# Kernel optimization log

Hardware: AMD Instinct MI355X
Metric: run time of the kernel (lower is better)

## Reference

```python
import jax, jax.numpy as jnp
import numpy as np

NUM_GRAPHS = 512
EPS = 1e-5

def squash(x):
    # capsule squash: (|x|^2 / (1 + |x|^2)) * x / |x|
    n2 = jnp.sum(x * x, axis=-1, keepdims=True)
    return (n2 / (1.0 + n2)) * x * jax.lax.rsqrt(n2 + 1e-12)

def setup_inputs():
    key = jax.random.key(0)
    ks = jax.random.split(key, 16)
    N, E, F, H, L, C = 100000, 600000, 128, 128, 3, 2
    x = jax.random.normal(ks[0], (N, F), jnp.float32)
    edge_index = jax.random.randint(ks[1], (2, E), 0, N)
    batch = jnp.sort(jax.random.randint(ks[2], (N,), 0, NUM_GRAPHS))
    def lin(k, i, o):
        return (jax.random.normal(k, (i, o), jnp.float32) / np.sqrt(i)).astype(jnp.float32)
    return {
        'x': x, 'edge_index': edge_index, 'batch': batch,
        'bn_gamma': jnp.ones((F,), jnp.float32), 'bn_beta': jnp.zeros((F,), jnp.float32),
        'W0': lin(ks[3], F, H), 'b0': jnp.zeros((H,), jnp.float32),
        'W1': lin(ks[4], H, H), 'b1': jnp.zeros((H,), jnp.float32),
        'W2': lin(ks[5], H, H), 'b2': jnp.zeros((H,), jnp.float32),
        'tar_w': (jax.random.normal(ks[6], (L, H), jnp.float32) / np.sqrt(H)).astype(jnp.float32),
        'lin1_w': lin(ks[7], 3 * H, H), 'lin1_b': jnp.zeros((H,), jnp.float32),
        'lin2_w': lin(ks[8], H, C), 'lin2_b': jnp.zeros((C,), jnp.float32),
    }

def reference(x, edge_index, batch, bn_gamma, bn_beta, W0, b0, W1, b1, W2, b2,
              tar_w, lin1_w, lin1_b, lin2_w, lin2_b):
    N, G = x.shape[0], NUM_GRAPHS
    # input BatchNorm1d (training-mode batch statistics)
    mu = jnp.mean(x, 0)
    var = jnp.var(x, 0)
    h = (x - mu) * jax.lax.rsqrt(var + EPS) * bn_gamma + bn_beta
    # remove_self_loops + add_remaining_self_loops ~= append diagonal with weight 1
    loops = jnp.arange(N)
    src = jnp.concatenate([edge_index[0], loops])
    dst = jnp.concatenate([edge_index[1], loops])
    w = jnp.ones((src.shape[0],), h.dtype)
    # GCN symmetric normalization D^-1/2 A D^-1/2
    deg = jax.ops.segment_sum(w, dst, num_segments=N)
    dinv = jax.lax.rsqrt(jnp.maximum(deg, 1e-12))
    norm = dinv[src] * w * dinv[dst]  # [E+N]
    ones_n = jnp.ones((N,), h.dtype)
    cnt = jax.ops.segment_sum(ones_n, batch, num_segments=G)  # nodes per graph
    cnt_safe = jnp.maximum(cnt, 1.0)[:, None]
    graph_rep = jnp.zeros((G, 3 * W0.shape[1]), h.dtype)
    loss_stability = jnp.zeros((), h.dtype)
    for i, (W, b) in enumerate([(W0, b0), (W1, b1), (W2, b2)]):
        m = h @ W  # [N, H]
        agg = jax.ops.segment_sum(norm[:, None] * m[src], dst, num_segments=N) + b
        h = squash(agg)
        loss_stability = loss_stability + jnp.mean((agg - h) ** 2)
        # Task-Aware Readout: node attention then fused sum / mean / max scatters
        attn = h @ tar_w[i]  # [N]
        x_wsum = jax.ops.segment_sum(attn[:, None] * h, batch, num_segments=G)
        x_mean = jax.ops.segment_sum(h, batch, num_segments=G) / cnt_safe
        x_max = jax.ops.segment_max(h, batch, num_segments=G)
        x_max = jnp.where(cnt[:, None] > 0, x_max, 0.0)
        graph_rep = graph_rep + jnp.concatenate([x_wsum, x_mean, x_max], axis=-1)
    z = jax.nn.relu(graph_rep @ lin1_w + lin1_b)
    z = z @ lin2_w + lin2_b
    return jax.nn.log_softmax(z, axis=-1)
```

## Files before the change

kernel.cpp:

```cpp
#include <hip/hip_runtime.h>
#include <hip/hip_bf16.h>
#include <math.h>

#define BN_EPS 1e-5f
#define NCHUNK 256

typedef __attribute__((ext_vector_type(8)))  short short8v;
typedef __attribute__((ext_vector_type(16))) float f32x16;

__device__ __forceinline__ unsigned short f2bf(float f){
  union { float f; unsigned u; } v; v.f = f;
  unsigned r = v.u + 0x7FFFu + ((v.u >> 16) & 1u);
  return (unsigned short)(r >> 16);
}
__device__ __forceinline__ float2 bfpair(unsigned u){
  union { unsigned u; float f; } lo, hi;
  lo.u = u << 16;
  hi.u = u & 0xFFFF0000u;
  return make_float2(lo.f, hi.f);
}
__device__ __forceinline__ unsigned packbf(float a, float b){
  return (unsigned)f2bf(a) | ((unsigned)f2bf(b) << 16);
}

__global__ __launch_bounds__(256) void k_hist_bn(const int* __restrict__ dst,
                                                 int* __restrict__ hist2, int E, int NB, int CH,
                                                 const float* __restrict__ x,
                                                 float* __restrict__ part, int total4){
  int tid = threadIdx.x;
  if (blockIdx.x < NCHUNK){
    __shared__ int lh[512];
    for (int i = tid; i < NB; i += 256) lh[i] = 0;
    __syncthreads();
    int c = blockIdx.x;
    int e0 = c*CH, e1 = min(e0 + CH, E);
    for (int e = e0 + tid; e < e1; e += 256)
      atomicAdd(&lh[dst[e] >> 8], 1);
    __syncthreads();
    for (int i = tid; i < NB; i += 256)
      hist2[c*NB + i] = lh[i];
  } else {
    const float4* x4 = (const float4*)x;
    int bb = blockIdx.x - NCHUNK;
    int stride = 512 * 256;
    float4 s = make_float4(0.f,0.f,0.f,0.f);
    float4 q = make_float4(0.f,0.f,0.f,0.f);
    for (int idx = bb*256 + tid; idx < total4; idx += stride){
      float4 v = x4[idx];
      s.x += v.x; s.y += v.y; s.z += v.z; s.w += v.w;
      q.x += v.x*v.x; q.y += v.y*v.y; q.z += v.z*v.z; q.w += v.w*v.w;
    }
    __shared__ float4 shs[256], shq[256];
    shs[tid] = s; shq[tid] = q;
    __syncthreads();
    if (tid < 32){
      int c4 = tid;
      float4 ts = shs[c4], tq = shq[c4];
      #pragma unroll
      for (int j = 1; j < 8; ++j){
        float4 os = shs[c4 + j*32], oq = shq[c4 + j*32];
        ts.x += os.x; ts.y += os.y; ts.z += os.z; ts.w += os.w;
        tq.x += oq.x; tq.y += oq.y; tq.z += oq.z; tq.w += oq.w;
      }
      float* pb = part + (size_t)bb * 256;
      *(float4*)(pb + c4*4)       = ts;
      *(float4*)(pb + 128 + c4*4) = tq;
    }
  }
}

__global__ __launch_bounds__(512) void k_scan_red_gb(const int* __restrict__ hist2,
                                                     int* __restrict__ offs2,
                                                     int* __restrict__ bbase, int NB, int E,
                                                     const float* __restrict__ part,
                                                     const float* __restrict__ gamma,
                                                     const float* __restrict__ beta,
                                                     float* __restrict__ scale,
                                                     float* __restrict__ shift, int N,
                                                     const int* __restrict__ batch,
                                                     int* __restrict__ gstart, int G){
  int t = threadIdx.x;
  if (blockIdx.x == 0){
    __shared__ int tot[512];
    int b = t;
    int total = 0;
    if (b < NB){
      for (int c = 0; c < NCHUNK; c += 8){
        int h0 = hist2[(c+0)*NB + b], h1 = hist2[(c+1)*NB + b];
        int h2 = hist2[(c+2)*NB + b], h3 = hist2[(c+3)*NB + b];
        int h4 = hist2[(c+4)*NB + b], h5 = hist2[(c+5)*NB + b];
        int h6 = hist2[(c+6)*NB + b], h7 = hist2[(c+7)*NB + b];
        total += ((h0+h1)+(h2+h3)) + ((h4+h5)+(h6+h7));
      }
    }
    tot[b] = (b < NB) ? total : 0;
    __syncthreads();
    int v = tot[b];
    for (int d = 1; d < 512; d <<= 1){
      int u = (b >= d) ? tot[b-d] : 0;
      __syncthreads();
      tot[b] += u;
      __syncthreads();
    }
    if (b < NB){
      int base = tot[b] - v;
      bbase[b] = base;
      int run = base;
      for (int c = 0; c < NCHUNK; ++c){
        offs2[c*NB + b] = run;
        run += hist2[c*NB + b];
      }
    }
    if (b == 0) bbase[NB] = E;
  } else if (blockIdx.x == 1){
    if (t < 256){
      float a0=0.f,a1=0.f,a2=0.f,a3=0.f,a4=0.f,a5=0.f,a6=0.f,a7=0.f;
      for (int b = 0; b < 512; b += 8){
        a0 += part[(size_t)(b+0)*256 + t];
        a1 += part[(size_t)(b+1)*256 + t];
        a2 += part[(size_t)(b+2)*256 + t];
        a3 += part[(size_t)(b+3)*256 + t];
        a4 += part[(size_t)(b+4)*256 + t];
        a5 += part[(size_t)(b+5)*256 + t];
        a6 += part[(size_t)(b+6)*256 + t];
        a7 += part[(size_t)(b+7)*256 + t];
      }
      float acc = ((a0+a1)+(a2+a3)) + ((a4+a5)+(a6+a7));
      __shared__ float sh[256];
      sh[t] = acc;
      __syncthreads();
      if (t < 128){
        float mu  = sh[t] / (float)N;
        float var = sh[t+128] / (float)N - mu*mu;
        float sc  = gamma[t] * rsqrtf(var + BN_EPS);
        scale[t] = sc;
        shift[t] = beta[t] - mu*sc;
      }
    }
  } else {
    int g = (blockIdx.x - 2)*512 + t;
    if (g <= G){
      int lo = 0, hi = N;
      while (lo < hi){ int mid = (lo+hi)>>1; if (batch[mid] < g) lo = mid+1; else hi = mid; }
      gstart[g] = lo;
    }
  }
}

__global__ __launch_bounds__(256) void chunk_scatter(const int* __restrict__ src,
                                                     const int* __restrict__ dst,
                                                     const int* __restrict__ offs2,
                                                     unsigned* __restrict__ ebuf,
                                                     int E, int NB, int CH){
  __shared__ int lcur[512];
  int c = blockIdx.x;
  for (int i = threadIdx.x; i < NB; i += 256) lcur[i] = offs2[c*NB + i];
  __syncthreads();
  int e0 = c*CH, e1 = min(e0 + CH, E);
  for (int e = e0 + threadIdx.x; e < e1; e += 256){
    int d = dst[e];
    int b = d >> 8;
    int pos = atomicAdd(&lcur[b], 1);
    ebuf[pos] = ((unsigned)(d & 255) << 24) | (unsigned)src[e];
  }
}

__global__ __launch_bounds__(256) void k_sort_prep(const unsigned* __restrict__ ebuf,
                                                   const int* __restrict__ bbase,
                                                   int* __restrict__ csrs,
                                                   int* __restrict__ rowstart,
                                                   float* __restrict__ dinv,
                                                   int N, int E, int NB,
                                                   const float* __restrict__ W0,
                                                   const float* __restrict__ W1,
                                                   const float* __restrict__ W2,
                                                   const float* __restrict__ scale,
                                                   unsigned short* __restrict__ Wh,
                                                   const float* __restrict__ b0,
                                                   const float* __restrict__ shift,
                                                   float* __restrict__ bias0p){
  int tid = threadIdx.x;
  if ((int)blockIdx.x < NB){
    int b = blockIdx.x;
    int base = bbase[b];
    int end  = bbase[b+1];
    int len  = end - base;
    __shared__ int cnt[256];
    __shared__ int pref[256];
    cnt[tid] = 0;
    __syncthreads();
    for (int i = tid; i < len; i += 256)
      atomicAdd(&cnt[ebuf[base + i] >> 24], 1);
    __syncthreads();
    int v = cnt[tid];
    pref[tid] = v;
    __syncthreads();
    for (int d = 1; d < 256; d <<= 1){
      int u = (tid >= d) ? pref[tid-d] : 0;
      __syncthreads();
      pref[tid] += u;
      __syncthreads();
    }
    int excl = pref[tid] - v;
    int node = b*256 + tid;
    if (node < N){
      rowstart[node] = base + excl;
      dinv[node] = rsqrtf((float)v + 1.0f);
    }
    cnt[tid] = excl;
    __syncthreads();
    for (int i = tid; i < len; i += 256){
      unsigned r = ebuf[base + i];
      int pos = atomicAdd(&cnt[r >> 24], 1);
      csrs[base + pos] = (int)(r & 0xFFFFFFu);
    }
    if (b == NB-1 && tid == 0) rowstart[N] = E;
  } else if ((int)blockIdx.x < NB + 192){
    int idx = (blockIdx.x - NB)*256 + tid;
    int l = idx >> 14, r = idx & 16383, c = r >> 7, k = r & 127;
    const float* W = (l==0) ? W0 : (l==1) ? W1 : W2;
    float v = W[k*128 + c];
    if (l == 0) v *= scale[k];
    Wh[idx] = f2bf(v);
  } else {
    __shared__ float sh[128];
    if (tid < 128) sh[tid] = shift[tid];
    __syncthreads();
    if (tid < 128){
      float s = b0[tid];
      for (int c = 0; c < 128; ++c) s += sh[c] * W0[c*128 + tid];
      bias0p[tid] = s;
    }
  }
}

template<int CVT>
__global__ __launch_bounds__(512) void gemm_mfma(
    const float* __restrict__ A32, const unsigned short* __restrict__ A16,
    const unsigned short* __restrict__ Bh, unsigned short* __restrict__ C, int N){
  __shared__ unsigned short Ah[64*128];
  int tid = threadIdx.x;
  int r0 = blockIdx.x * 64;
  int w = tid >> 6, lane = tid & 63;
  int rt = w & 1;
  int ct = (w >> 1) * 32;
  int lrow = 32*rt + (lane & 31);
  int khalf = lane >> 5;
  int c0 = ct + (lane & 31);
  const unsigned short* bh0 = Bh + (size_t)c0*128 + khalf*8;

  short8v bhf[8];
  #pragma unroll
  for (int s = 0; s < 8; ++s) bhf[s] = *(const short8v*)(bh0 + s*16);

  if (CVT){
    #pragma unroll
    for (int it = 0; it < 4; ++it){
      int idx = tid + it*512;
      int row = idx >> 5;
      int c4  = idx & 31;
      int r = r0 + row;
      float4 av = (r < N) ? *(const float4*)(A32 + (size_t)r*128 + c4*4)
                          : make_float4(0.f,0.f,0.f,0.f);
      int byte0 = (c4*8) ^ ((row & 15) << 4);
      uint2 p = make_uint2(packbf(av.x, av.y), packbf(av.z, av.w));
      *(uint2*)((char*)Ah + row*256 + byte0) = p;
    }
  } else {
    #pragma unroll
    for (int it = 0; it < 2; ++it){
      int idx = tid + it*512;
      int row = idx >> 4;
      int c8  = idx & 15;
      int r = r0 + row;
      uint4 v = (r < N) ? *(const uint4*)(A16 + (size_t)r*128 + c8*8)
                        : make_uint4(0,0,0,0);
      int byte0 = (c8*16) ^ ((row & 15) << 4);
      *(uint4*)((char*)Ah + row*256 + byte0) = v;
    }
  }
  __syncthreads();

  f32x16 acc = {};
  const char* AhB = (const char*)Ah + lrow*256;
  int sw = (lrow & 15) << 4;
  #pragma unroll
  for (int s = 0; s < 8; ++s){
    int abyte = (s*32 + khalf*16) ^ sw;
    short8v a = *(const short8v*)(AhB + abyte);
    acc = __builtin_amdgcn_mfma_f32_32x32x16_bf16(a, bhf[s], acc, 0, 0, 0);
  }

  #pragma unroll
  for (int r = 0; r < 16; ++r){
    int row = r0 + 32*rt + (r & 3) + 8*(r >> 2) + 4*khalf;
    if (row < N) C[(size_t)row*128 + c0] = f2bf(acc[r]);
  }
}

__global__ __launch_bounds__(256) void gather_squash(
    const unsigned short* __restrict__ m, const int* __restrict__ rowstart,
    const int* __restrict__ csrs, const float* __restrict__ dinv,
    const float* __restrict__ bias, const float* __restrict__ tar,
    unsigned short* __restrict__ h, float* __restrict__ attn, int N){
  int node = blockIdx.x*8 + (threadIdx.x >> 5);
  if (node >= N) return;
  int lane = threadIdx.x & 31;
  const uint2* m2 = (const uint2*)m;
  float dv = dinv[node];
  float sn = dv*dv;
  uint2 sv = m2[(size_t)node*32 + lane];
  float2 p0 = bfpair(sv.x), p1 = bfpair(sv.y);
  float a0 = p0.x*sn, a1 = p0.y*sn, a2 = p1.x*sn, a3 = p1.y*sn;
  int j0 = rowstart[node], j1 = rowstart[node+1];

  for (int base = j0; base < j1; base += 32){
    int cnt = j1 - base; if (cnt > 32) cnt = 32;
    int sidx = 0; float swt = 0.f;
    if (lane < cnt){
      sidx = csrs[base + lane];
      swt  = dinv[sidx] * dv;
    }
    int t = 0;
    for (; t + 4 <= cnt; t += 4){
      int s0 = __shfl(sidx, t, 32),   s1 = __shfl(sidx, t+1, 32);
      int s2 = __shfl(sidx, t+2, 32), s3 = __shfl(sidx, t+3, 32);
      float w0 = __shfl(swt, t, 32),   w1 = __shfl(swt, t+1, 32);
      float w2 = __shfl(swt, t+2, 32), w3 = __shfl(swt, t+3, 32);
      uint2 u0 = m2[(size_t)s0*32 + lane];
      uint2 u1 = m2[(size_t)s1*32 + lane];
      uint2 u2 = m2[(size_t)s2*32 + lane];
      uint2 u3 = m2[(size_t)s3*32 + lane];
      float2 q0, q1;
      q0 = bfpair(u0.x); q1 = bfpair(u0.y);
      a0 += w0*q0.x; a1 += w0*q0.y; a2 += w0*q1.x; a3 += w0*q1.y;
      q0 = bfpair(u1.x); q1 = bfpair(u1.y);
      a0 += w1*q0.x; a1 += w1*q0.y; a2 += w1*q1.x; a3 += w1*q1.y;
      q0 = bfpair(u2.x); q1 = bfpair(u2.y);
      a0 += w2*q0.x; a1 += w2*q0.y; a2 += w2*q1.x; a3 += w2*q1.y;
      q0 = bfpair(u3.x); q1 = bfpair(u3.y);
      a0 += w3*q0.x; a1 += w3*q0.y; a2 += w3*q1.x; a3 += w3*q1.y;
    }
    if (cnt - t >= 2){
      int s0 = __shfl(sidx, t, 32), s1 = __shfl(sidx, t+1, 32);
      float w0 = __shfl(swt, t, 32), w1 = __shfl(swt, t+1, 32);
      uint2 u0 = m2[(size_t)s0*32 + lane];
      uint2 u1 = m2[(size_t)s1*32 + lane];
      float2 q0 = bfpair(u0.x), q1 = bfpair(u0.y);
      a0 += w0*q0.x; a1 += w0*q0.y; a2 += w0*q1.x; a3 += w0*q1.y;
      q0 = bfpair(u1.x); q1 = bfpair(u1.y);
      a0 += w1*q0.x; a1 += w1*q0.y; a2 += w1*q1.x; a3 += w1*q1.y;
      t += 2;
    }
    if (t < cnt){
      int s0 = __shfl(sidx, t, 32);
      float w0 = __shfl(swt, t, 32);
      uint2 u0 = m2[(size_t)s0*32 + lane];
      float2 q0 = bfpair(u0.x), q1 = bfpair(u0.y);
      a0 += w0*q0.x; a1 += w0*q0.y; a2 += w0*q1.x; a3 += w0*q1.y;
    }
  }

  float4 bv = ((const float4*)bias)[lane];
  a0 += bv.x; a1 += bv.y; a2 += bv.z; a3 += bv.w;
  float n2 = a0*a0 + a1*a1 + a2*a2 + a3*a3;
  #pragma unroll
  for (int o = 16; o > 0; o >>= 1) n2 += __shfl_xor(n2, o);
  float sc = (n2/(1.f+n2)) * rsqrtf(n2 + 1e-12f);
  float h0 = a0*sc, h1 = a1*sc, h2 = a2*sc, h3 = a3*sc;
  ((uint2*)(h + (size_t)node*128))[lane] = make_uint2(packbf(h0,h1), packbf(h2,h3));
  float4 tv = ((const float4*)tar)[lane];
  float at = h0*tv.x + h1*tv.y + h2*tv.z + h3*tv.w;
  #pragma unroll
  for (int o = 16; o > 0; o >>= 1) at += __shfl_xor(at, o);
  if (lane == 0) attn[node] = at;
}

__global__ __launch_bounds__(1024) void readout(const unsigned short* __restrict__ h,
                                                const float* __restrict__ attn,
                                                const int* __restrict__ gstart,
                                                float* __restrict__ grep){
  int g = blockIdx.x;
  int t   = threadIdx.x & 63;
  int grp = threadIdx.x >> 6;
  int a = gstart[g], b = gstart[g+1];
  float wsx = 0.f, wsy = 0.f, smx_ = 0.f, smy_ = 0.f;
  float mxx = -INFINITY, mxy = -INFINITY;
  for (int n = a + grp; n < b; n += 16){
    unsigned u = ((const unsigned*)(h + (size_t)n*128))[t];
    float2 v = bfpair(u);
    float at = attn[n];
    wsx += at*v.x; wsy += at*v.y;
    smx_ += v.x;  smy_ += v.y;
    mxx = fmaxf(mxx, v.x); mxy = fmaxf(mxy, v.y);
  }
  __shared__ float2 sws[16][64], ssm[16][64], smx[16][64];
  sws[grp][t] = make_float2(wsx, wsy);
  ssm[grp][t] = make_float2(smx_, smy_);
  smx[grp][t] = make_float2(mxx, mxy);
  __syncthreads();
  if (grp == 0){
    #pragma unroll
    for (int j = 1; j < 16; ++j){
      float2 ow = sws[j][t], os = ssm[j][t], om = smx[j][t];
      wsx += ow.x; wsy += ow.y;
      smx_ += os.x; smy_ += os.y;
      mxx = fmaxf(mxx, om.x); mxy = fmaxf(mxy, om.y);
    }
    int cnt = b - a;
    float inv = 1.f / fmaxf((float)cnt, 1.f);
    if (cnt == 0){ mxx = 0.f; mxy = 0.f; }
    grep[(size_t)g*384 + t*2]           += wsx;
    grep[(size_t)g*384 + t*2 + 1]       += wsy;
    grep[(size_t)g*384 + 128 + t*2]     += smx_*inv;
    grep[(size_t)g*384 + 128 + t*2 + 1] += smy_*inv;
    grep[(size_t)g*384 + 256 + t*2]     += mxx;
    grep[(size_t)g*384 + 256 + t*2 + 1] += mxy;
  }
}

__global__ __launch_bounds__(128) void classify(const float* __restrict__ grep,
                                                const float* __restrict__ w1, const float* __restrict__ b1,
                                                const float* __restrict__ w2, const float* __restrict__ b2,
                                                float* __restrict__ out){
  int g = blockIdx.x, t = threadIdx.x;
  __shared__ float gr[384];
  for (int i = t; i < 384; i += 128) gr[i] = grep[(size_t)g*384 + i];
  __syncthreads();
  float z = b1[t];
  for (int k = 0; k < 384; ++k) z += gr[k]*w1[k*128 + t];
  z = fmaxf(z, 0.f);
  float c0 = z*w2[t*2 + 0], c1 = z*w2[t*2 + 1];
  #pragma unroll
  for (int o = 32; o > 0; o >>= 1){ c0 += __shfl_xor(c0, o); c1 += __shfl_xor(c1, o); }
  __shared__ float r0s[2], r1s[2];
  if ((t & 63) == 0){ r0s[t>>6] = c0; r1s[t>>6] = c1; }
  __syncthreads();
  if (t == 0){
    float z0 = r0s[0] + r0s[1] + b2[0];
    float z1 = r1s[0] + r1s[1] + b2[1];
    float mm = fmaxf(z0, z1);
    float lse = mm + logf(expf(z0-mm) + expf(z1-mm));
    out[g*2 + 0] = z0 - lse;
    out[g*2 + 1] = z1 - lse;
  }
}

extern "C" void kernel_launch(void* const* d_in, const int* in_sizes, int n_in,
                              void* d_out, int out_size, void* d_ws, size_t ws_size,
                              hipStream_t stream) {
  const float* x     = (const float*)d_in[0];
  const int*   ei    = (const int*)d_in[1];
  const int*   batch = (const int*)d_in[2];
  const float* gamma = (const float*)d_in[3];
  const float* beta  = (const float*)d_in[4];
  const float* W0    = (const float*)d_in[5];
  const float* b0    = (const float*)d_in[6];
  const float* W1    = (const float*)d_in[7];
  const float* b1    = (const float*)d_in[8];
  const float* W2    = (const float*)d_in[9];
  const float* b2    = (const float*)d_in[10];
  const float* tar   = (const float*)d_in[11];
  const float* l1w   = (const float*)d_in[12];
  const float* l1b   = (const float*)d_in[13];
  const float* l2w   = (const float*)d_in[14];
  const float* l2b   = (const float*)d_in[15];
  float* out = (float*)d_out;

  int N = in_sizes[0] / 128;
  int E = in_sizes[1] / 2;
  int G = out_size / 2;
  const int* srcp = ei;
  const int* dstp = ei + E;

  char* wsb = (char*)d_ws;
  size_t off = 0;
  auto alloc = [&](size_t bytes)->char*{
    char* p = wsb + off; off += (bytes + 255) & ~(size_t)255; return p;
  };
  unsigned short* h = (unsigned short*)alloc((size_t)N*128*2);
  unsigned short* m = (unsigned short*)alloc((size_t)N*128*2);
  float* attn    = (float*)alloc((size_t)N*4);
  float* dinv    = (float*)alloc((size_t)N*4);
  int*   rowst   = (int*)  alloc((size_t)(N+1)*4);
  int*   csrs    = (int*)  alloc((size_t)E*4);
  unsigned* ebuf = (unsigned*)alloc((size_t)E*4);
  int*   hist2   = (int*)  alloc((size_t)NCHUNK*512*4);
  int*   offs2   = (int*)  alloc((size_t)NCHUNK*512*4);
  int*   bbase   = (int*)  alloc(513*4);
  int*   gstart  = (int*)  alloc((size_t)(G+1)*4);
  float* grep    = (float*)alloc((size_t)G*384*4);
  float* stats   = (float*)alloc(2*128*4);
  float* bias0p  = (float*)alloc(128*4);
  float* part    = (float*)alloc((size_t)512*256*4);
  unsigned short* Wh = (unsigned short*)alloc(3*16384*2);
  (void)ws_size;

  float* scale  = stats;
  float* shift  = stats + 128;

  int NB = (N + 255) >> 8;
  int CH = (E + NCHUNK - 1) / NCHUNK;
  hipMemsetAsync(grep, 0, (size_t)G*384*4, stream);

  k_hist_bn<<<NCHUNK + 512, 256, 0, stream>>>(dstp, hist2, E, NB, CH, x, part, N*32);
  k_scan_red_gb<<<4, 512, 0, stream>>>(hist2, offs2, bbase, NB, E,
                                       part, gamma, beta, scale, shift, N,
                                       batch, gstart, G);
  chunk_scatter<<<NCHUNK, 256, 0, stream>>>(srcp, dstp, offs2, ebuf, E, NB, CH);
  k_sort_prep<<<NB + 193, 256, 0, stream>>>(ebuf, bbase, csrs, rowst, dinv, N, E, NB,
                                            W0, W1, W2, scale, Wh, b0, shift, bias0p);

  const float* bs[3] = {bias0p, b1, b2};
  int nb64 = (N + 63) / 64;
  for (int l = 0; l < 3; ++l){
    if (l == 0)
      gemm_mfma<1><<<nb64, 512, 0, stream>>>(x, nullptr, Wh, m, N);
    else
      gemm_mfma<0><<<nb64, 512, 0, stream>>>(nullptr, h, Wh + l*16384, m, N);
    gather_squash<<<(N+7)/8, 256, 0, stream>>>(m, rowst, csrs, dinv, bs[l], tar + l*128, h, attn, N);
    readout<<<G, 1024, 0, stream>>>(h, attn, gstart, grep);
  }
  classify<<<G, 128, 0, stream>>>(grep, l1w, l1b, l2w, l2b, out);
}
```

Baseline: 252.4 us.

## Merge independent kernels into shared launches to cut launch count

Launches that do not depend on each other now share one kernel and branch on block index. The grep memset moves into the histogram/BN kernel, and the weight conversion joins chunk_scatter. The CSR sort runs in the same launch as the layer-0 GEMM, and each readout is fused with the next layer's GEMM. This removes several launches and lets independent work overlap, at the cost of mixed block types, larger shared memory per block, and an 8-group readout instead of 16.

```diff
diff --git a/kernel.cpp b/kernel.cpp
--- a/kernel.cpp
+++ b/kernel.cpp
@@ -23,10 +23,157 @@
   return (unsigned)f2bf(a) | ((unsigned)f2bf(b) << 16);
 }
 
-__global__ __launch_bounds__(256) void k_hist_bn(const int* __restrict__ dst,
-                                                 int* __restrict__ hist2, int E, int NB, int CH,
-                                                 const float* __restrict__ x,
-                                                 float* __restrict__ part, int total4){
+
+template<int CVT>
+__device__ __forceinline__ void gemm_body(int bid, int tid,
+    const float* __restrict__ A32, const unsigned short* __restrict__ A16,
+    const unsigned short* __restrict__ Bh, unsigned short* __restrict__ C, int N,
+    unsigned short* Ah){
+  int r0 = bid * 64;
+  int w = tid >> 6, lane = tid & 63;
+  int rt = w & 1;
+  int ct = (w >> 1) * 32;
+  int lrow = 32*rt + (lane & 31);
+  int khalf = lane >> 5;
+  int c0 = ct + (lane & 31);
+  const unsigned short* bh0 = Bh + (size_t)c0*128 + khalf*8;
+
+  short8v bhf[8];
+  #pragma unroll
+  for (int s = 0; s < 8; ++s) bhf[s] = *(const short8v*)(bh0 + s*16);
+
+  if (CVT){
+    #pragma unroll
+    for (int it = 0; it < 4; ++it){
+      int idx = tid + it*512;
+      int row = idx >> 5;
+      int c4  = idx & 31;
+      int r = r0 + row;
+      float4 av = (r < N) ? *(const float4*)(A32 + (size_t)r*128 + c4*4)
+                          : make_float4(0.f,0.f,0.f,0.f);
+      int byte0 = (c4*8) ^ ((row & 15) << 4);
+      uint2 p = make_uint2(packbf(av.x, av.y), packbf(av.z, av.w));
+      *(uint2*)((char*)Ah + row*256 + byte0) = p;
+    }
+  } else {
+    #pragma unroll
+    for (int it = 0; it < 2; ++it){
+      int idx = tid + it*512;
+      int row = idx >> 4;
+      int c8  = idx & 15;
+      int r = r0 + row;
+      uint4 v = (r < N) ? *(const uint4*)(A16 + (size_t)r*128 + c8*8)
+                        : make_uint4(0,0,0,0);
+      int byte0 = (c8*16) ^ ((row & 15) << 4);
+      *(uint4*)((char*)Ah + row*256 + byte0) = v;
+    }
+  }
+  __syncthreads();
+
+  f32x16 acc = {};
+  const char* AhB = (const char*)Ah + lrow*256;
+  int sw = (lrow & 15) << 4;
+  #pragma unroll
+  for (int s = 0; s < 8; ++s){
+    int abyte = (s*32 + khalf*16) ^ sw;
+    short8v a = *(const short8v*)(AhB + abyte);
+    acc = __builtin_amdgcn_mfma_f32_32x32x16_bf16(a, bhf[s], acc, 0, 0, 0);
+  }
+
+  #pragma unroll
+  for (int r = 0; r < 16; ++r){
+    int row = r0 + 32*rt + (r & 3) + 8*(r >> 2) + 4*khalf;
+    if (row < N) C[(size_t)row*128 + c0] = f2bf(acc[r]);
+  }
+}
+
+__device__ __forceinline__ void readout_body(int g, int tid,
+    const unsigned short* __restrict__ h, const float* __restrict__ attn,
+    const int* __restrict__ gstart, float* __restrict__ grep, char* smem){
+  float2* sws = (float2*)smem;
+  float2* ssm = sws + 8*64;
+  float2* smx = ssm + 8*64;
+  int t = tid & 63, grp = tid >> 6;
+  int a = gstart[g], b = gstart[g+1];
+  float wsx = 0.f, wsy = 0.f, smx_ = 0.f, smy_ = 0.f;
+  float mxx = -INFINITY, mxy = -INFINITY;
+  for (int n = a + grp; n < b; n += 8){
+    unsigned u = ((const unsigned*)(h + (size_t)n*128))[t];
+    float2 v = bfpair(u);
+    float at = attn[n];
+    wsx += at*v.x; wsy += at*v.y;
+    smx_ += v.x;  smy_ += v.y;
+    mxx = fmaxf(mxx, v.x); mxy = fmaxf(mxy, v.y);
+  }
+  sws[grp*64 + t] = make_float2(wsx, wsy);
+  ssm[grp*64 + t] = make_float2(smx_, smy_);
+  smx[grp*64 + t] = make_float2(mxx, mxy);
+  __syncthreads();
+  if (grp == 0){
+    #pragma unroll
+    for (int j = 1; j < 8; ++j){
+      float2 ow = sws[j*64 + t], os = ssm[j*64 + t], om = smx[j*64 + t];
+      wsx += ow.x; wsy += ow.y;
+      smx_ += os.x; smy_ += os.y;
+      mxx = fmaxf(mxx, om.x); mxy = fmaxf(mxy, om.y);
+    }
+    int cnt = b - a;
+    float inv = 1.f / fmaxf((float)cnt, 1.f);
+    if (cnt == 0){ mxx = 0.f; mxy = 0.f; }
+    grep[(size_t)g*384 + t*2]           += wsx;
+    grep[(size_t)g*384 + t*2 + 1]       += wsy;
+    grep[(size_t)g*384 + 128 + t*2]     += smx_*inv;
+    grep[(size_t)g*384 + 128 + t*2 + 1] += smy_*inv;
+    grep[(size_t)g*384 + 256 + t*2]     += mxx;
+    grep[(size_t)g*384 + 256 + t*2 + 1] += mxy;
+  }
+}
+
+__device__ __forceinline__ void sort_body(int b, int tid,
+    const unsigned* __restrict__ ebuf, const int* __restrict__ bbase,
+    int* __restrict__ csrs, int* __restrict__ rowstart, float* __restrict__ dinv,
+    int N, int E, int NB, int* cnt, int* pref){
+  bool act = tid < 256;
+  int base = bbase[b], end = bbase[b+1], len = end - base;
+  if (act) cnt[tid] = 0;
+  __syncthreads();
+  if (act) for (int i = tid; i < len; i += 256)
+    atomicAdd(&cnt[ebuf[base + i] >> 24], 1);
+  __syncthreads();
+  int v = 0;
+  if (act){ v = cnt[tid]; pref[tid] = v; }
+  __syncthreads();
+  for (int d = 1; d < 256; d <<= 1){
+    int u = 0;
+    if (act && tid >= d) u = pref[tid-d];
+    __syncthreads();
+    if (act) pref[tid] += u;
+    __syncthreads();
+  }
+  if (act){
+    int excl = pref[tid] - v;
+    int node = b*256 + tid;
+    if (node < N){
+      rowstart[node] = base + excl;
+      dinv[node] = rsqrtf((float)v + 1.0f);
+    }
+    cnt[tid] = excl;
+  }
+  __syncthreads();
+  if (act) for (int i = tid; i < len; i += 256){
+    unsigned r = ebuf[base + i];
+    int pos = atomicAdd(&cnt[r >> 24], 1);
+    csrs[base + pos] = (int)(r & 0xFFFFFFu);
+  }
+  if (b == NB-1 && tid == 0) rowstart[N] = E;
+}
+
+
+__global__ __launch_bounds__(256) void k_pre1(const int* __restrict__ dst,
+                                              int* __restrict__ hist2, int E, int NB, int CH,
+                                              const float* __restrict__ x,
+                                              float* __restrict__ part, int total4,
+                                              float* __restrict__ grep, int zt4){
   int tid = threadIdx.x;
   if (blockIdx.x < NCHUNK){
     __shared__ int lh[512];
@@ -39,7 +186,7 @@
     __syncthreads();
     for (int i = tid; i < NB; i += 256)
       hist2[c*NB + i] = lh[i];
-  } else {
+  } else if (blockIdx.x < NCHUNK + 512){
     const float4* x4 = (const float4*)x;
     int bb = blockIdx.x - NCHUNK;
     int stride = 512 * 256;
@@ -66,19 +213,25 @@
       *(float4*)(pb + c4*4)       = ts;
       *(float4*)(pb + 128 + c4*4) = tq;
     }
-  }
-}
-
-__global__ __launch_bounds__(512) void k_scan_red_gb(const int* __restrict__ hist2,
-                                                     int* __restrict__ offs2,
-                                                     int* __restrict__ bbase, int NB, int E,
-                                                     const float* __restrict__ part,
-                                                     const float* __restrict__ gamma,
-                                                     const float* __restrict__ beta,
-                                                     float* __restrict__ scale,
-                                                     float* __restrict__ shift, int N,
-                                                     const int* __restrict__ batch,
-                                                     int* __restrict__ gstart, int G){
+  } else {
+    float4* g4 = (float4*)grep;
+    int bb = blockIdx.x - NCHUNK - 512;
+    int stride = 24 * 256;
+    float4 z = make_float4(0.f,0.f,0.f,0.f);
+    for (int idx = bb*256 + tid; idx < zt4; idx += stride) g4[idx] = z;
+  }
+}
+
+__global__ __launch_bounds__(512) void k_pre2(const int* __restrict__ hist2,
+                                              int* __restrict__ offs2,
+                                              int* __restrict__ bbase, int NB, int E,
+                                              const float* __restrict__ part,
+                                              const float* __restrict__ gamma,
+                                              const float* __restrict__ beta,
+                                              float* __restrict__ scale,
+                                              float* __restrict__ shift, int N,
+                                              const int* __restrict__ batch,
+                                              int* __restrict__ gstart, int G){
   int t = threadIdx.x;
   if (blockIdx.x == 0){
     __shared__ int tot[512];
@@ -147,83 +300,62 @@
   }
 }
 
-__global__ __launch_bounds__(256) void chunk_scatter(const int* __restrict__ src,
-                                                     const int* __restrict__ dst,
-                                                     const int* __restrict__ offs2,
-                                                     unsigned* __restrict__ ebuf,
-                                                     int E, int NB, int CH){
-  __shared__ int lcur[512];
-  int c = blockIdx.x;
-  for (int i = threadIdx.x; i < NB; i += 256) lcur[i] = offs2[c*NB + i];
-  __syncthreads();
-  int e0 = c*CH, e1 = min(e0 + CH, E);
-  for (int e = e0 + threadIdx.x; e < e1; e += 256){
-    int d = dst[e];
-    int b = d >> 8;
-    int pos = atomicAdd(&lcur[b], 1);
-    ebuf[pos] = ((unsigned)(d & 255) << 24) | (unsigned)src[e];
-  }
-}
-
-__global__ __launch_bounds__(256) void k_sort_prep(const unsigned* __restrict__ ebuf,
-                                                   const int* __restrict__ bbase,
-                                                   int* __restrict__ csrs,
-                                                   int* __restrict__ rowstart,
-                                                   float* __restrict__ dinv,
-                                                   int N, int E, int NB,
-                                                   const float* __restrict__ W0,
-                                                   const float* __restrict__ W1,
-                                                   const float* __restrict__ W2,
-                                                   const float* __restrict__ scale,
-                                                   unsigned short* __restrict__ Wh,
-                                                   const float* __restrict__ b0,
-                                                   const float* __restrict__ shift,
-                                                   float* __restrict__ bias0p){
+__global__ __launch_bounds__(256) void k_pre3(const int* __restrict__ src,
+                                              const int* __restrict__ dst,
+                                              const int* __restrict__ offs2,
+                                              unsigned* __restrict__ ebuf,
+                                              int E, int NB, int CH,
+                                              const float* __restrict__ W0,
+                                              const float* __restrict__ W1,
+                                              const float* __restrict__ W2,
+                                              const float* __restrict__ scale,
+                                              unsigned short* __restrict__ Wh){
   int tid = threadIdx.x;
-  if ((int)blockIdx.x < NB){
-    int b = blockIdx.x;
-    int base = bbase[b];
-    int end  = bbase[b+1];
-    int len  = end - base;
-    __shared__ int cnt[256];
-    __shared__ int pref[256];
-    cnt[tid] = 0;
-    __syncthreads();
-    for (int i = tid; i < len; i += 256)
-      atomicAdd(&cnt[ebuf[base + i] >> 24], 1);
-    __syncthreads();
-    int v = cnt[tid];
-    pref[tid] = v;
-    __syncthreads();
-    for (int d = 1; d < 256; d <<= 1){
-      int u = (tid >= d) ? pref[tid-d] : 0;
-      __syncthreads();
-      pref[tid] += u;
-      __syncthreads();
-    }
-    int excl = pref[tid] - v;
-    int node = b*256 + tid;
-    if (node < N){
-      rowstart[node] = base + excl;
-      dinv[node] = rsqrtf((float)v + 1.0f);
-    }
-    cnt[tid] = excl;
-    __syncthreads();
-    for (int i = tid; i < len; i += 256){
-      unsigned r = ebuf[base + i];
-      int pos = atomicAdd(&cnt[r >> 24], 1);
-      csrs[base + pos] = (int)(r & 0xFFFFFFu);
-    }
-    if (b == NB-1 && tid == 0) rowstart[N] = E;
-  } else if ((int)blockIdx.x < NB + 192){
-    int idx = (blockIdx.x - NB)*256 + tid;
+  if (blockIdx.x < NCHUNK){
+    __shared__ int lcur[512];
+    int c = blockIdx.x;
+    for (int i = tid; i < NB; i += 256) lcur[i] = offs2[c*NB + i];
+    __syncthreads();
+    int e0 = c*CH, e1 = min(e0 + CH, E);
+    for (int e = e0 + tid; e < e1; e += 256){
+      int d = dst[e];
+      int b = d >> 8;
+      int pos = atomicAdd(&lcur[b], 1);
+      ebuf[pos] = ((unsigned)(d & 255) << 24) | (unsigned)src[e];
+    }
+  } else {
+    int idx = (blockIdx.x - NCHUNK)*256 + tid;
     int l = idx >> 14, r = idx & 16383, c = r >> 7, k = r & 127;
     const float* W = (l==0) ? W0 : (l==1) ? W1 : W2;
     float v = W[k*128 + c];
     if (l == 0) v *= scale[k];
     Wh[idx] = f2bf(v);
+  }
+}
+
+__global__ __launch_bounds__(512) void k_sort_gemm0(const unsigned* __restrict__ ebuf,
+                                                    const int* __restrict__ bbase,
+                                                    int* __restrict__ csrs,
+                                                    int* __restrict__ rowstart,
+                                                    float* __restrict__ dinv,
+                                                    int N, int E, int NB, int nb64,
+                                                    const float* __restrict__ b0,
+                                                    const float* __restrict__ shift,
+                                                    const float* __restrict__ W0,
+                                                    float* __restrict__ bias0p,
+                                                    const float* __restrict__ x,
+                                                    const unsigned short* __restrict__ Wh,
+                                                    unsigned short* __restrict__ m){
+  __shared__ float4 smem4[1024];
+  int tid = threadIdx.x;
+  if ((int)blockIdx.x < nb64){
+    gemm_body<1>(blockIdx.x, tid, x, nullptr, Wh, m, N, (unsigned short*)smem4);
+  } else if ((int)blockIdx.x < nb64 + NB){
+    int* cnt = (int*)smem4;
+    int* pref = cnt + 256;
+    sort_body(blockIdx.x - nb64, tid, ebuf, bbase, csrs, rowstart, dinv, N, E, NB, cnt, pref);
   } else {
-    __shared__ float sh[128];
+    float* sh = (float*)smem4;
     if (tid < 128) sh[tid] = shift[tid];
     __syncthreads();
     if (tid < 128){
@@ -234,67 +366,18 @@
   }
 }
 
-template<int CVT>
-__global__ __launch_bounds__(512) void gemm_mfma(
-    const float* __restrict__ A32, const unsigned short* __restrict__ A16,
-    const unsigned short* __restrict__ Bh, unsigned short* __restrict__ C, int N){
-  __shared__ unsigned short Ah[64*128];
-  int tid = threadIdx.x;
-  int r0 = blockIdx.x * 64;
-  int w = tid >> 6, lane = tid & 63;
-  int rt = w & 1;
-  int ct = (w >> 1) * 32;
-  int lrow = 32*rt + (lane & 31);
-  int khalf = lane >> 5;
-  int c0 = ct + (lane & 31);
-  const unsigned short* bh0 = Bh + (size_t)c0*128 + khalf*8;
-
-  short8v bhf[8];
-  #pragma unroll
-  for (int s = 0; s < 8; ++s) bhf[s] = *(const short8v*)(bh0 + s*16);
-
-  if (CVT){
-    #pragma unroll
-    for (int it = 0; it < 4; ++it){
-      int idx = tid + it*512;
-      int row = idx >> 5;
-      int c4  = idx & 31;
-      int r = r0 + row;
-      float4 av = (r < N) ? *(const float4*)(A32 + (size_t)r*128 + c4*4)
-                          : make_float4(0.f,0.f,0.f,0.f);
-      int byte0 = (c4*8) ^ ((row & 15) << 4);
-      uint2 p = make_uint2(packbf(av.x, av.y), packbf(av.z, av.w));
-      *(uint2*)((char*)Ah + row*256 + byte0) = p;
-    }
+__global__ __launch_bounds__(512) void k_ro_gemm(const unsigned short* __restrict__ h,
+                                                 const float* __restrict__ attn,
+                                                 const int* __restrict__ gstart,
+                                                 float* __restrict__ grep,
+                                                 const unsigned short* __restrict__ Bh,
+                                                 unsigned short* __restrict__ m,
+                                                 int N, int nb64){
+  __shared__ float4 smem4[1024];
+  if ((int)blockIdx.x < nb64){
+    gemm_body<0>(blockIdx.x, threadIdx.x, nullptr, h, Bh, m, N, (unsigned short*)smem4);
   } else {
-    #pragma unroll
-    for (int it = 0; it < 2; ++it){
-      int idx = tid + it*512;
-      int row = idx >> 4;
-      int c8  = idx & 15;
-      int r = r0 + row;
-      uint4 v = (r < N) ? *(const uint4*)(A16 + (size_t)r*128 + c8*8)
-                        : make_uint4(0,0,0,0);
-      int byte0 = (c8*16) ^ ((row & 15) << 4);
-      *(uint4*)((char*)Ah + row*256 + byte0) = v;
-    }
-  }
-  __syncthreads();
-
-  f32x16 acc = {};
-  const char* AhB = (const char*)Ah + lrow*256;
-  int sw = (lrow & 15) << 4;
-  #pragma unroll
-  for (int s = 0; s < 8; ++s){
-    int abyte = (s*32 + khalf*16) ^ sw;
-    short8v a = *(const short8v*)(AhB + abyte);
-    acc = __builtin_amdgcn_mfma_f32_32x32x16_bf16(a, bhf[s], acc, 0, 0, 0);
-  }
-
-  #pragma unroll
-  for (int r = 0; r < 16; ++r){
-    int row = r0 + 32*rt + (r & 3) + 8*(r >> 2) + 4*khalf;
-    if (row < N) C[(size_t)row*128 + c0] = f2bf(acc[r]);
+    readout_body(blockIdx.x - nb64, threadIdx.x, h, attn, gstart, grep, (char*)smem4);
   }
 }
 
@@ -374,49 +457,6 @@
   #pragma unroll
   for (int o = 16; o > 0; o >>= 1) at += __shfl_xor(at, o);
   if (lane == 0) attn[node] = at;
-}
-
-__global__ __launch_bounds__(1024) void readout(const unsigned short* __restrict__ h,
-                                                const float* __restrict__ attn,
-                                                const int* __restrict__ gstart,
-                                                float* __restrict__ grep){
-  int g = blockIdx.x;
-  int t   = threadIdx.x & 63;
-  int grp = threadIdx.x >> 6;
-  int a = gstart[g], b = gstart[g+1];
-  float wsx = 0.f, wsy = 0.f, smx_ = 0.f, smy_ = 0.f;
-  float mxx = -INFINITY, mxy = -INFINITY;
-  for (int n = a + grp; n < b; n += 16){
-    unsigned u = ((const unsigned*)(h + (size_t)n*128))[t];
-    float2 v = bfpair(u);
-    float at = attn[n];
-    wsx += at*v.x; wsy += at*v.y;
-    smx_ += v.x;  smy_ += v.y;
-    mxx = fmaxf(mxx, v.x); mxy = fmaxf(mxy, v.y);
-  }
-  __shared__ float2 sws[16][64], ssm[16][64], smx[16][64];
-  sws[grp][t] = make_float2(wsx, wsy);
-  ssm[grp][t] = make_float2(smx_, smy_);
-  smx[grp][t] = make_float2(mxx, mxy);
-  __syncthreads();
-  if (grp == 0){
-    #pragma unroll
-    for (int j = 1; j < 16; ++j){
-      float2 ow = sws[j][t], os = ssm[j][t], om = smx[j][t];
-      wsx += ow.x; wsy += ow.y;
-      smx_ += os.x; smy_ += os.y;
-      mxx = fmaxf(mxx, om.x); mxy = fmaxf(mxy, om.y);
-    }
-    int cnt = b - a;
-    float inv = 1.f / fmaxf((float)cnt, 1.f);
-    if (cnt == 0){ mxx = 0.f; mxy = 0.f; }
-    grep[(size_t)g*384 + t*2]           += wsx;
-    grep[(size_t)g*384 + t*2 + 1]       += wsy;
-    grep[(size_t)g*384 + 128 + t*2]     += smx_*inv;
-    grep[(size_t)g*384 + 128 + t*2 + 1] += smy_*inv;
-    grep[(size_t)g*384 + 256 + t*2]     += mxx;
-    grep[(size_t)g*384 + 256 + t*2 + 1] += mxy;
-  }
 }
 
 __global__ __launch_bounds__(128) void classify(const float* __restrict__ grep,
@@ -501,25 +541,22 @@
 
   int NB = (N + 255) >> 8;
   int CH = (E + NCHUNK - 1) / NCHUNK;
-  hipMemsetAsync(grep, 0, (size_t)G*384*4, stream);
-
-  k_hist_bn<<<NCHUNK + 512, 256, 0, stream>>>(dstp, hist2, E, NB, CH, x, part, N*32);
-  k_scan_red_gb<<<4, 512, 0, stream>>>(hist2, offs2, bbase, NB, E,
-                                       part, gamma, beta, scale, shift, N,
-                                       batch, gstart, G);
-  chunk_scatter<<<NCHUNK, 256, 0, stream>>>(srcp, dstp, offs2, ebuf, E, NB, CH);
-  k_sort_prep<<<NB + 193, 256, 0, stream>>>(ebuf, bbase, csrs, rowst, dinv, N, E, NB,
-                                            W0, W1, W2, scale, Wh, b0, shift, bias0p);
-
-  const float* bs[3] = {bias0p, b1, b2};
   int nb64 = (N + 63) / 64;
-  for (int l = 0; l < 3; ++l){
-    if (l == 0)
-      gemm_mfma<1><<<nb64, 512, 0, stream>>>(x, nullptr, Wh, m, N);
-    else
-      gemm_mfma<0><<<nb64, 512, 0, stream>>>(nullptr, h, Wh + l*16384, m, N);
-    gather_squash<<<(N+7)/8, 256, 0, stream>>>(m, rowst, csrs, dinv, bs[l], tar + l*128, h, attn, N);
-    readout<<<G, 1024, 0, stream>>>(h, attn, gstart, grep);
-  }
+  int zt4 = (G*384) / 4;
+
+  k_pre1<<<NCHUNK + 512 + 24, 256, 0, stream>>>(dstp, hist2, E, NB, CH, x, part, N*32, grep, zt4);
+  k_pre2<<<4, 512, 0, stream>>>(hist2, offs2, bbase, NB, E,
+                                part, gamma, beta, scale, shift, N, batch, gstart, G);
+  k_pre3<<<NCHUNK + 192, 256, 0, stream>>>(srcp, dstp, offs2, ebuf, E, NB, CH,
+                                           W0, W1, W2, scale, Wh);
+  k_sort_gemm0<<<nb64 + NB + 1, 512, 0, stream>>>(ebuf, bbase, csrs, rowst, dinv,
+                                                  N, E, NB, nb64, b0, shift, W0, bias0p,
+                                                  x, Wh, m);
+  gather_squash<<<(N+7)/8, 256, 0, stream>>>(m, rowst, csrs, dinv, bias0p, tar, h, attn, N);
+  k_ro_gemm<<<nb64 + G, 512, 0, stream>>>(h, attn, gstart, grep, Wh + 16384, m, N, nb64);
+  gather_squash<<<(N+7)/8, 256, 0, stream>>>(m, rowst, csrs, dinv, b1, tar + 128, h, attn, N);
+  k_ro_gemm<<<nb64 + G, 512, 0, stream>>>(h, attn, gstart, grep, Wh + 2*16384, m, N, nb64);
+  gather_squash<<<(N+7)/8, 256, 0, stream>>>(m, rowst, csrs, dinv, b2, tar + 256, h, attn, N);
+  k_ro_gemm<<<G, 512, 0, stream>>>(h, attn, gstart, grep, Wh, m, N, 0);
   classify<<<G, 128, 0, stream>>>(grep, l1w, l1b, l2w, l2b, out);
 }
```

After: 242.4 us. 3.9% less time.
